# Kernel optimization log

Hardware: AMD Instinct MI355X
Metric: run time of the kernel (lower is better)

## Reference

```python
import jax, jax.numpy as jnp
import numpy as np

ALPHA = 2.0  # snntorch ATan surrogate default alpha
BATCH = 500_000
NUM_STEPS = 32

@jax.custom_vjp
def spike(x):
    # Heaviside forward, ATan surrogate backward (snntorch default)
    return (x > 0).astype(x.dtype)

def _spike_fwd(x):
    return (x > 0).astype(x.dtype), x

def _spike_bwd(x, g):
    return (g * (ALPHA / 2.0) / (1.0 + (jnp.pi / 2.0 * ALPHA * x) ** 2),)

spike.defvjp(_spike_fwd, _spike_bwd)


def setup_inputs() -> dict:
    key = jax.random.key(0)
    ks = jax.random.split(key, 5)
    inv_sqrt2 = 1.0 / np.sqrt(2.0)
    return {
        "x": jax.random.normal(ks[0], (BATCH, 2), dtype=jnp.float32),
        "fc1_w": jax.random.uniform(ks[1], (2, 2), dtype=jnp.float32, minval=0.0, maxval=2.0),
        "fc1_b": jax.random.uniform(ks[2], (2,), dtype=jnp.float32, minval=-inv_sqrt2, maxval=inv_sqrt2),
        "beta1": jnp.full((1,), 0.5, dtype=jnp.float32),
        "thr1": jnp.ones((1,), dtype=jnp.float32),
        "fc2_w": jax.random.uniform(ks[3], (2, 2), dtype=jnp.float32, minval=-1.0, maxval=3.0),
        "fc2_b": jax.random.uniform(ks[4], (2,), dtype=jnp.float32, minval=-inv_sqrt2, maxval=inv_sqrt2),
        "beta2": jnp.full((1,), 0.5, dtype=jnp.float32),
        "thr2": jnp.ones((1,), dtype=jnp.float32),
        "num_steps": NUM_STEPS,
    }


def reference(x, fc1_w, fc1_b, beta1, thr1, fc2_w, fc2_b, beta2, thr2, num_steps):
    # dynamic_input=False: cur1 is the same every timestep
    cur1 = x @ fc1_w.T + fc1_b  # [B, 2]
    b1 = jnp.clip(beta1, 0.0, 1.0)
    b2 = jnp.clip(beta2, 0.0, 1.0)

    def step(carry, _):
        mem1, mem2 = carry
        # reset computed from previous mem, detached (snntorch mem_reset)
        reset1 = jax.lax.stop_gradient((mem1 - thr1 > 0).astype(mem1.dtype))
        mem1 = b1 * mem1 + cur1 - reset1 * thr1
        spk1 = spike(mem1 - thr1)
        cur2 = spk1 @ fc2_w.T + fc2_b
        reset2 = jax.lax.stop_gradient((mem2 - thr2 > 0).astype(mem2.dtype))
        mem2 = b2 * mem2 + cur2 - reset2 * thr2
        spk2 = spike(mem2 - thr2)
        return (mem1, mem2), (spk1, spk2, mem2)

    init = (jnp.zeros_like(cur1), jnp.zeros_like(cur1))
    _, (spk1_rec, spk2_rec, mem2_rec) = jax.lax.scan(step, init, None, length=num_steps)
    # [T, B, 2] each, matching torch.stack(..., dim=0)
    return spk1_rec, spk2_rec, mem2_rec
```

## Files before the change

kernel.cpp:

```cpp
#include <hip/hip_runtime.h>


typedef float floatv4 __attribute__((ext_vector_type(4)));

__global__ __launch_bounds__(256) void snn_fwd_kernel(
    const float* __restrict__ x,
    const float* __restrict__ fc1_w,
    const float* __restrict__ fc1_b,
    const float* __restrict__ beta1,
    const float* __restrict__ thr1,
    const float* __restrict__ fc2_w,
    const float* __restrict__ fc2_b,
    const float* __restrict__ beta2,
    const float* __restrict__ thr2,
    float* __restrict__ out,
    int B2, int T)
{
#pragma clang fp contract(off)
    int tid = blockIdx.x * blockDim.x + threadIdx.x;
    if (tid >= B2) return;

    const floatv4 xv = ((const floatv4*)x)[tid];

    const float w00 = fc1_w[0], w01 = fc1_w[1], w10 = fc1_w[2], w11 = fc1_w[3];
    const float ca0 = (xv.x * w00 + xv.y * w01) + fc1_b[0];
    const float ca1 = (xv.x * w10 + xv.y * w11) + fc1_b[1];
    const float cb0 = (xv.z * w00 + xv.w * w01) + fc1_b[0];
    const float cb1 = (xv.z * w10 + xv.w * w11) + fc1_b[1];

    const float b1 = fminf(fmaxf(beta1[0], 0.0f), 1.0f);
    const float b2 = fminf(fmaxf(beta2[0], 0.0f), 1.0f);
    const float t1 = thr1[0];
    const float t2 = thr2[0];

    const float v00 = fc2_w[0], v01 = fc2_w[1], v10 = fc2_w[2], v11 = fc2_w[3];
    const float fb0 = fc2_b[0], fb1 = fc2_b[1];

    float m1a0 = 0.f, m1a1 = 0.f, m1b0 = 0.f, m1b1 = 0.f;
    float m2a0 = 0.f, m2a1 = 0.f, m2b0 = 0.f, m2b1 = 0.f;

    const size_t TB2 = (size_t)T * (size_t)B2;
    floatv4* __restrict__ spk1_out = (floatv4*)out;
    floatv4* __restrict__ spk2_out = (floatv4*)out + TB2;
    floatv4* __restrict__ mem2_out = (floatv4*)out + 2 * TB2;

    size_t off = (size_t)tid;
    for (int t = 0; t < T; ++t, off += (size_t)B2) {
        const float r1a0 = ((m1a0 - t1) > 0.f) ? 1.f : 0.f;
        const float r1a1 = ((m1a1 - t1) > 0.f) ? 1.f : 0.f;
        const float r1b0 = ((m1b0 - t1) > 0.f) ? 1.f : 0.f;
        const float r1b1 = ((m1b1 - t1) > 0.f) ? 1.f : 0.f;
        m1a0 = (b1 * m1a0 + ca0) - r1a0 * t1;
        m1a1 = (b1 * m1a1 + ca1) - r1a1 * t1;
        m1b0 = (b1 * m1b0 + cb0) - r1b0 * t1;
        m1b1 = (b1 * m1b1 + cb1) - r1b1 * t1;
        const float s1a0 = ((m1a0 - t1) > 0.f) ? 1.f : 0.f;
        const float s1a1 = ((m1a1 - t1) > 0.f) ? 1.f : 0.f;
        const float s1b0 = ((m1b0 - t1) > 0.f) ? 1.f : 0.f;
        const float s1b1 = ((m1b1 - t1) > 0.f) ? 1.f : 0.f;
        const float c2a0 = (s1a0 * v00 + s1a1 * v01) + fb0;
        const float c2a1 = (s1a0 * v10 + s1a1 * v11) + fb1;
        const float c2b0 = (s1b0 * v00 + s1b1 * v01) + fb0;
        const float c2b1 = (s1b0 * v10 + s1b1 * v11) + fb1;
        const float r2a0 = ((m2a0 - t2) > 0.f) ? 1.f : 0.f;
        const float r2a1 = ((m2a1 - t2) > 0.f) ? 1.f : 0.f;
        const float r2b0 = ((m2b0 - t2) > 0.f) ? 1.f : 0.f;
        const float r2b1 = ((m2b1 - t2) > 0.f) ? 1.f : 0.f;
        m2a0 = (b2 * m2a0 + c2a0) - r2a0 * t2;
        m2a1 = (b2 * m2a1 + c2a1) - r2a1 * t2;
        m2b0 = (b2 * m2b0 + c2b0) - r2b0 * t2;
        m2b1 = (b2 * m2b1 + c2b1) - r2b1 * t2;
        const float s2a0 = ((m2a0 - t2) > 0.f) ? 1.f : 0.f;
        const float s2a1 = ((m2a1 - t2) > 0.f) ? 1.f : 0.f;
        const float s2b0 = ((m2b0 - t2) > 0.f) ? 1.f : 0.f;
        const float s2b1 = ((m2b1 - t2) > 0.f) ? 1.f : 0.f;

        floatv4 o1; o1.x = s1a0; o1.y = s1a1; o1.z = s1b0; o1.w = s1b1;
        floatv4 o2; o2.x = s2a0; o2.y = s2a1; o2.z = s2b0; o2.w = s2b1;
        floatv4 o3; o3.x = m2a0; o3.y = m2a1; o3.z = m2b0; o3.w = m2b1;
        spk1_out[off] = o1;
        spk2_out[off] = o2;
        mem2_out[off] = o3;
    }
}

extern "C" void kernel_launch(void* const* d_in, const int* in_sizes, int n_in,
                              void* d_out, int out_size, void* d_ws, size_t ws_size,
                              hipStream_t stream) {
    const float* x      = (const float*)d_in[0];
    const float* fc1_w  = (const float*)d_in[1];
    const float* fc1_b  = (const float*)d_in[2];
    const float* beta1  = (const float*)d_in[3];
    const float* thr1   = (const float*)d_in[4];
    const float* fc2_w  = (const float*)d_in[5];
    const float* fc2_b  = (const float*)d_in[6];
    const float* beta2  = (const float*)d_in[7];
    const float* thr2   = (const float*)d_in[8];
    float* out = (float*)d_out;

    const int B  = in_sizes[0] / 2;
    const int T  = out_size / (6 * B);
    const int B2 = B / 2;

    const int block = 256;
    const int grid = (B2 + block - 1) / block;
    snn_fwd_kernel<<<grid, block, 0, stream>>>(x, fc1_w, fc1_b, beta1, thr1,
                                               fc2_w, fc2_b, beta2, thr2,
                                               out, B2, T);
}
```

Baseline: 392.6 us.

## Split output streams across three block roles to triple parallelism

Launches three times as many blocks. Each block takes one role: role 0 writes spk1, role 1 writes spk2 and role 2 writes mem2. Each role recomputes only the recurrence it needs, so every thread issues one store stream instead of three. The aim is more waves in flight and less store pressure per thread, which should help saturate write bandwidth on this store-bound kernel. The cost is redundant recomputation of the layer-1 and layer-2 recurrence and three reads of x.

New measurement: 399.1 us. Within noise of the previous version (+1.6%).

```diff
diff --git a/kernel.cpp b/kernel.cpp
--- a/kernel.cpp
+++ b/kernel.cpp
@@ -17,7 +17,9 @@
     int B2, int T)
 {
 #pragma clang fp contract(off)
-    int tid = blockIdx.x * blockDim.x + threadIdx.x;
+    const int bid  = blockIdx.x;
+    const int role = bid % 3;
+    const int tid  = (bid / 3) * blockDim.x + threadIdx.x;
     if (tid >= B2) return;
 
     const floatv4 xv = ((const floatv4*)x)[tid];
@@ -29,22 +31,45 @@
     const float cb1 = (xv.z * w10 + xv.w * w11) + fc1_b[1];
 
     const float b1 = fminf(fmaxf(beta1[0], 0.0f), 1.0f);
+    const float t1 = thr1[0];
+
+    float m1a0 = 0.f, m1a1 = 0.f, m1b0 = 0.f, m1b1 = 0.f;
+
+    const size_t TB2 = (size_t)T * (size_t)B2;
+    size_t off = (size_t)tid;
+
+    if (role == 0) {
+        floatv4* __restrict__ o = (floatv4*)out;
+        for (int t = 0; t < T; ++t, off += (size_t)B2) {
+            const float r1a0 = ((m1a0 - t1) > 0.f) ? 1.f : 0.f;
+            const float r1a1 = ((m1a1 - t1) > 0.f) ? 1.f : 0.f;
+            const float r1b0 = ((m1b0 - t1) > 0.f) ? 1.f : 0.f;
+            const float r1b1 = ((m1b1 - t1) > 0.f) ? 1.f : 0.f;
+            m1a0 = (b1 * m1a0 + ca0) - r1a0 * t1;
+            m1a1 = (b1 * m1a1 + ca1) - r1a1 * t1;
+            m1b0 = (b1 * m1b0 + cb0) - r1b0 * t1;
+            m1b1 = (b1 * m1b1 + cb1) - r1b1 * t1;
+            const float s1a0 = ((m1a0 - t1) > 0.f) ? 1.f : 0.f;
+            const float s1a1 = ((m1a1 - t1) > 0.f) ? 1.f : 0.f;
+            const float s1b0 = ((m1b0 - t1) > 0.f) ? 1.f : 0.f;
+            const float s1b1 = ((m1b1 - t1) > 0.f) ? 1.f : 0.f;
+            floatv4 o1; o1.x = s1a0; o1.y = s1a1; o1.z = s1b0; o1.w = s1b1;
+            o[off] = o1;
+        }
+        return;
+    }
+
     const float b2 = fminf(fmaxf(beta2[0], 0.0f), 1.0f);
-    const float t1 = thr1[0];
     const float t2 = thr2[0];
-
     const float v00 = fc2_w[0], v01 = fc2_w[1], v10 = fc2_w[2], v11 = fc2_w[3];
     const float fb0 = fc2_b[0], fb1 = fc2_b[1];
 
-    float m1a0 = 0.f, m1a1 = 0.f, m1b0 = 0.f, m1b1 = 0.f;
     float m2a0 = 0.f, m2a1 = 0.f, m2b0 = 0.f, m2b1 = 0.f;
 
-    const size_t TB2 = (size_t)T * (size_t)B2;
-    floatv4* __restrict__ spk1_out = (floatv4*)out;
-    floatv4* __restrict__ spk2_out = (floatv4*)out + TB2;
-    floatv4* __restrict__ mem2_out = (floatv4*)out + 2 * TB2;
+    floatv4* __restrict__ o = (role == 1) ? ((floatv4*)out + TB2)
+                                          : ((floatv4*)out + 2 * TB2);
+    const bool store_spk = (role == 1);
 
-    size_t off = (size_t)tid;
     for (int t = 0; t < T; ++t, off += (size_t)B2) {
         const float r1a0 = ((m1a0 - t1) > 0.f) ? 1.f : 0.f;
         const float r1a1 = ((m1a1 - t1) > 0.f) ? 1.f : 0.f;
@@ -70,17 +95,17 @@
         m2a1 = (b2 * m2a1 + c2a1) - r2a1 * t2;
         m2b0 = (b2 * m2b0 + c2b0) - r2b0 * t2;
         m2b1 = (b2 * m2b1 + c2b1) - r2b1 * t2;
-        const float s2a0 = ((m2a0 - t2) > 0.f) ? 1.f : 0.f;
-        const float s2a1 = ((m2a1 - t2) > 0.f) ? 1.f : 0.f;
-        const float s2b0 = ((m2b0 - t2) > 0.f) ? 1.f : 0.f;
-        const float s2b1 = ((m2b1 - t2) > 0.f) ? 1.f : 0.f;
 
-        floatv4 o1; o1.x = s1a0; o1.y = s1a1; o1.z = s1b0; o1.w = s1b1;
-        floatv4 o2; o2.x = s2a0; o2.y = s2a1; o2.z = s2b0; o2.w = s2b1;
-        floatv4 o3; o3.x = m2a0; o3.y = m2a1; o3.z = m2b0; o3.w = m2b1;
-        spk1_out[off] = o1;
-        spk2_out[off] = o2;
-        mem2_out[off] = o3;
+        floatv4 ov;
+        if (store_spk) {
+            ov.x = ((m2a0 - t2) > 0.f) ? 1.f : 0.f;
+            ov.y = ((m2a1 - t2) > 0.f) ? 1.f : 0.f;
+            ov.z = ((m2b0 - t2) > 0.f) ? 1.f : 0.f;
+            ov.w = ((m2b1 - t2) > 0.f) ? 1.f : 0.f;
+        } else {
+            ov.x = m2a0; ov.y = m2a1; ov.z = m2b0; ov.w = m2b1;
+        }
+        o[off] = ov;
     }
 }
 
@@ -103,7 +128,8 @@
     const int B2 = B / 2;
 
     const int block = 256;
-    const int grid = (B2 + block - 1) / block;
+    const int blocksPerRole = (B2 + block - 1) / block;
+    const int grid = 3 * blocksPerRole;
     snn_fwd_kernel<<<grid, block, 0, stream>>>(x, fc1_w, fc1_b, beta1, thr1,
                                                fc2_w, fc2_b, beta2, thr2,
                                                out, B2, T);
```
